# Kernel tuning notes

Hardware: AMD Instinct MI355X
Metric: run time of the kernel (lower is better)

Reference implementation:

```python
import jax, jax.numpy as jnp
import numpy as np

B, S, HID = 1, 2048, 3072
NH, NKV, HD = 24, 8, 128
ROT = 96
OP = NH * HD + 2 * NKV * HD
MASK_VALUE = -jnp.finfo(jnp.float32).max


def setup_inputs() -> dict:
    key = jax.random.key(0)
    k1, k2, k3, k4, k5 = jax.random.split(key, 5)
    hidden_states = jax.random.normal(k1, (B, S, HID), dtype=jnp.float32)
    # rotary embeddings: use actual cos/sin of rope angles for realism
    inv_freq = 1.0 / (10000.0 ** (jnp.arange(0, ROT, 2, dtype=jnp.float32) / ROT))
    t = jnp.arange(S, dtype=jnp.float32)
    freqs = jnp.outer(t, inv_freq)  # [S, ROT/2]
    emb = jnp.concatenate([freqs, freqs], axis=-1)  # [S, ROT]
    cos = jnp.broadcast_to(jnp.cos(emb)[None], (B, S, ROT))
    sin = jnp.broadcast_to(jnp.sin(emb)[None], (B, S, ROT))
    attention_mask = jnp.ones((B, S), dtype=bool)
    w_qkv = jax.random.normal(k2, (OP, HID), dtype=jnp.float32) * (HID ** -0.5)
    w_o = jax.random.normal(k3, (HID, HID), dtype=jnp.float32) * (HID ** -0.5)
    return {"hidden_states": hidden_states, "cos": cos, "sin": sin,
            "attention_mask": attention_mask, "w_qkv": w_qkv, "w_o": w_o}


def rotate_half(x):
    x1, x2 = jnp.split(x, 2, axis=-1)
    return jnp.concatenate([-x2, x1], axis=-1)


def apply_rope(q, k, cos, sin):
    # cos/sin: [B, S, ROT] -> [B, 1, S, ROT]
    cos = cos[:, None]
    sin = sin[:, None]
    rd = cos.shape[-1]
    q_rot, q_pass = q[..., :rd], q[..., rd:]
    k_rot, k_pass = k[..., :rd], k[..., rd:]
    q = jnp.concatenate([q_rot * cos + rotate_half(q_rot) * sin, q_pass], axis=-1)
    k = jnp.concatenate([k_rot * cos + rotate_half(k_rot) * sin, k_pass], axis=-1)
    return q, k


def reference(hidden_states, cos, sin, attention_mask, w_qkv, w_o):
    b, n, _ = hidden_states.shape
    qkv = hidden_states @ w_qkv.T  # [B, S, OP]
    q, k, v = jnp.split(qkv, [NH * HD, NH * HD + NKV * HD], axis=-1)
    # b n (h d) -> b h n d
    q = q.reshape(b, n, NH, HD).transpose(0, 2, 1, 3)
    k = k.reshape(b, n, NKV, HD).transpose(0, 2, 1, 3)
    v = v.reshape(b, n, NKV, HD).transpose(0, 2, 1, 3)
    q, k = apply_rope(q, k, cos, sin)
    q = q * (HD ** -0.5)
    n_rep = NH // NKV
    if n_rep > 1:
        k = jnp.repeat(k, n_rep, axis=1)
        v = jnp.repeat(v, n_rep, axis=1)
    sim = jnp.einsum('bhid,bhjd->bhij', q, k)
    causal = jnp.triu(jnp.ones((n, n), dtype=bool), k=1)
    sim = jnp.where(causal, MASK_VALUE, sim)
    sim = jnp.where(~attention_mask[:, None, None, :], MASK_VALUE, sim)
    attn = jax.nn.softmax(sim.astype(jnp.float32), axis=-1).astype(v.dtype)
    out = jnp.einsum('bhij,bhjd->bhid', attn, v)
    out = out.transpose(0, 2, 1, 3).reshape(b, n, NH * HD)  # b h n d -> b n (h d)
    return out @ w_o.T
```

## Files before the change

kernel.cpp:

```cpp
#include <hip/hip_runtime.h>

typedef unsigned short u16;
typedef unsigned int u32;
typedef __bf16 bf16x8 __attribute__((ext_vector_type(8)));
typedef float f32x4 __attribute__((ext_vector_type(4)));

#define S_LEN 2048
#define HIDDEN 3072
#define NHEADS 24
#define NKVH 8
#define HDIM 128
#define QKVW 5120
#define QKLD 4096
#define PSTR 80

__device__ __forceinline__ u16 f2bf(float f) {
  u32 u = __float_as_uint(f);
  u32 r = (u + 0x7fffu + ((u >> 16) & 1u)) >> 16;
  return (u16)r;
}
__device__ __forceinline__ float bf2f(u16 h) { return __uint_as_float(((u32)h) << 16); }

__device__ __forceinline__ void gload_lds16(const void* g, void* l) {
  __builtin_amdgcn_global_load_lds((const __attribute__((address_space(1))) void*)g,
                                   (__attribute__((address_space(3))) void*)l, 16, 0, 0);
}

__global__ void cast4(const float4* __restrict__ in, uint2* __restrict__ out, int n4) {
  int i = blockIdx.x * blockDim.x + threadIdx.x;
  if (i >= n4) return;
  float4 f = in[i];
  uint2 o;
  o.x = ((u32)f2bf(f.y) << 16) | f2bf(f.x);
  o.y = ((u32)f2bf(f.w) << 16) | f2bf(f.z);
  out[i] = o;
}

__global__ __launch_bounds__(512, 2) void gemm256(const u16* __restrict__ A,
                                                  const u16* __restrict__ B,
                                                  u16* __restrict__ Cb,
                                                  u16* __restrict__ vtg) {
  __shared__ u16 lds[4][13312];
  const int tid = threadIdx.x;
  const int w = tid >> 6, lane = tid & 63;
  const int wm = w & 3, wn = w >> 2;
  const int l15 = lane & 15, qd = lane >> 4;
  const int K = 3072;
  const int m0 = ((int)blockIdx.x & 7) * 256;
  const int n0 = ((int)blockIdx.x >> 3) * 160;

  size_t offA[2], offB[2];
  int ldsA[2], ldsB[2];
#pragma unroll
  for (int it = 0; it < 2; ++it) {
    int CH = w * 128 + it * 64 + lane;
    int rp = CH >> 3, sl = CH & 7;
    int lin = sl ^ (rp & 7);
    int r = (rp << 1) | (lin >> 2), q = lin & 3;
    offA[it] = (size_t)(m0 + r) * K + q * 8;
    ldsA[it] = (w * 128 + it * 64) * 8;
  }
#pragma unroll
  for (int it = 0; it < 2; ++it) {
    int CH = it * 512 + w * 64 + lane;
    int rp = CH >> 3, sl = CH & 7;
    int lin = sl ^ (rp & 7);
    int r = (rp << 1) | (lin >> 2), q = lin & 3;
    offB[it] = (size_t)(n0 + r) * K + q * 8;
    ldsB[it] = 8192 + (it * 512 + w * 64) * 8;
  }

  int chA[4], chB[5];
#pragma unroll
  for (int i = 0; i < 4; ++i) {
    int r = wm * 64 + i * 16 + l15;
    chA[i] = ((r >> 1) * 8 + ((((r & 1) << 2) | qd) ^ ((r >> 1) & 7))) * 8;
  }
#pragma unroll
  for (int j = 0; j < 5; ++j) {
    int r = wn * 80 + j * 16 + l15;
    chB[j] = 8192 + ((r >> 1) * 8 + ((((r & 1) << 2) | qd) ^ ((r >> 1) & 7))) * 8;
  }

  f32x4 acc[4][5] = {};

  auto stage = [&](int s, int k0) {
    gload_lds16(A + offA[0] + k0, &lds[s][ldsA[0]]);
    gload_lds16(A + offA[1] + k0, &lds[s][ldsA[1]]);
    gload_lds16(B + offB[0] + k0, &lds[s][ldsB[0]]);
    if (w < 2) gload_lds16(B + offB[1] + k0, &lds[s][ldsB[1]]);
  };

  auto tile = [&](int s, int kpf, bool pf) {
    if (pf) stage((kpf >> 5) & 3, kpf);
    bf16x8 a[4], b[5];
#pragma unroll
    for (int i = 0; i < 4; ++i) a[i] = *(const bf16x8*)&lds[s][chA[i]];
#pragma unroll
    for (int j = 0; j < 5; ++j) b[j] = *(const bf16x8*)&lds[s][chB[j]];
    __builtin_amdgcn_s_setprio(1);
#pragma unroll
    for (int i = 0; i < 4; ++i)
#pragma unroll
      for (int j = 0; j < 5; ++j)
        acc[i][j] = __builtin_amdgcn_mfma_f32_16x16x32_bf16(a[i], b[j], acc[i][j], 0, 0, 0);
    __builtin_amdgcn_s_setprio(0);
  };

  stage(0, 0);
  stage(1, 32);
  stage(2, 64);
  if (w < 2) asm volatile("s_waitcnt vmcnt(8)" ::: "memory");
  else       asm volatile("s_waitcnt vmcnt(6)" ::: "memory");
  __builtin_amdgcn_s_barrier();

  for (int t = 0; t < 93; ++t) {
    tile(t & 3, (t + 3) * 32, true);
    if (w < 2) asm volatile("s_waitcnt vmcnt(8)" ::: "memory");
    else       asm volatile("s_waitcnt vmcnt(6)" ::: "memory");
    __builtin_amdgcn_s_barrier();
  }
  tile(1, 0, false);
  if (w < 2) asm volatile("s_waitcnt vmcnt(4)" ::: "memory");
  else       asm volatile("s_waitcnt vmcnt(3)" ::: "memory");
  __builtin_amdgcn_s_barrier();
  tile(2, 0, false);
  asm volatile("s_waitcnt vmcnt(0)" ::: "memory");
  __builtin_amdgcn_s_barrier();
  tile(3, 0, false);

#pragma unroll
  for (int j = 0; j < 5; ++j) {
    const int nf = n0 + wn * 80 + j * 16;
    if (nf >= 4096) {
#pragma unroll
      for (int i = 0; i < 4; ++i) {
        int nv = nf - 4096 + l15;
        int m = m0 + wm * 64 + i * 16 + qd * 4;
        uint2 p;
        p.x = ((u32)f2bf(acc[i][j][1]) << 16) | f2bf(acc[i][j][0]);
        p.y = ((u32)f2bf(acc[i][j][3]) << 16) | f2bf(acc[i][j][2]);
        *(uint2*)&vtg[(size_t)nv * S_LEN + m] = p;
      }
    } else {
#pragma unroll
      for (int i = 0; i < 4; ++i)
#pragma unroll
        for (int r = 0; r < 4; ++r) {
          int m = m0 + wm * 64 + i * 16 + qd * 4 + r;
          Cb[(size_t)m * QKLD + nf + l15] = f2bf(acc[i][j][r]);
        }
    }
  }
}

__global__ __launch_bounds__(512, 2) void gemm2k(const u16* __restrict__ A,
                                                 const u16* __restrict__ B,
                                                 float* __restrict__ C) {
  __shared__ u16 lds[4][10240];
  const int tid = threadIdx.x;
  const int w = tid >> 6, lane = tid & 63;
  const int wm = w & 1, wn = w >> 1;
  const int l15 = lane & 15, qd = lane >> 4;
  const int K = 3072;
  const int xcd = (int)blockIdx.x & 7, idx = (int)blockIdx.x >> 3;
  const int m0 = ((xcd & 1) * 8 + (idx & 7)) * 128;
  const int n0 = ((xcd >> 1) * 4 + (idx >> 3)) * 192;

  size_t offA, offB[2];
  int ldsAo, ldsB[2];
  {
    int CH = w * 64 + lane;
    int rp = CH >> 3, sl = CH & 7;
    int lin = sl ^ (rp & 7);
    int r = (rp << 1) | (lin >> 2), q = lin & 3;
    offA = (size_t)(m0 + r) * K + q * 8;
    ldsAo = (w * 64) * 8;
  }
#pragma unroll
  for (int it = 0; it < 2; ++it) {
    int CHb = (w < 4) ? (w * 128 + it * 64) : (512 + (w - 4) * 64);
    int CH = CHb + lane;
    int rp = CH >> 3, sl = CH & 7;
    int lin = sl ^ (rp & 7);
    int r = (rp << 1) | (lin >> 2), q = lin & 3;
    offB[it] = (size_t)(n0 + r) * K + q * 8;
    ldsB[it] = 4096 + CHb * 8;
  }

  int chA[4], chB[3];
#pragma unroll
  for (int i = 0; i < 4; ++i) {
    int r = wm * 64 + i * 16 + l15;
    chA[i] = ((r >> 1) * 8 + ((((r & 1) << 2) | qd) ^ ((r >> 1) & 7))) * 8;
  }
#pragma unroll
  for (int j = 0; j < 3; ++j) {
    int r = wn * 48 + j * 16 + l15;
    chB[j] = 4096 + ((r >> 1) * 8 + ((((r & 1) << 2) | qd) ^ ((r >> 1) & 7))) * 8;
  }

  f32x4 acc[4][3] = {};

  auto stage = [&](int s, int k0) {
    gload_lds16(A + offA + k0, &lds[s][ldsAo]);
    gload_lds16(B + offB[0] + k0, &lds[s][ldsB[0]]);
    if (w < 4) gload_lds16(B + offB[1] + k0, &lds[s][ldsB[1]]);
  };

  auto tile = [&](int s, int kpf, bool pf) {
    if (pf) stage((kpf >> 5) & 3, kpf);
    bf16x8 a[4], b[3];
#pragma unroll
    for (int i = 0; i < 4; ++i) a[i] = *(const bf16x8*)&lds[s][chA[i]];
#pragma unroll
    for (int j = 0; j < 3; ++j) b[j] = *(const bf16x8*)&lds[s][chB[j]];
    __builtin_amdgcn_s_setprio(1);
#pragma unroll
    for (int i = 0; i < 4; ++i)
#pragma unroll
      for (int j = 0; j < 3; ++j)
        acc[i][j] = __builtin_amdgcn_mfma_f32_16x16x32_bf16(a[i], b[j], acc[i][j], 0, 0, 0);
    __builtin_amdgcn_s_setprio(0);
  };

  stage(0, 0);
  stage(1, 32);
  stage(2, 64);
  if (w < 4) asm volatile("s_waitcnt vmcnt(6)" ::: "memory");
  else       asm volatile("s_waitcnt vmcnt(4)" ::: "memory");
  __builtin_amdgcn_s_barrier();

  for (int t = 0; t < 93; ++t) {
    tile(t & 3, (t + 3) * 32, true);
    if (w < 4) asm volatile("s_waitcnt vmcnt(6)" ::: "memory");
    else       asm volatile("s_waitcnt vmcnt(4)" ::: "memory");
    __builtin_amdgcn_s_barrier();
  }
  tile(1, 0, false);
  if (w < 4) asm volatile("s_waitcnt vmcnt(3)" ::: "memory");
  else       asm volatile("s_waitcnt vmcnt(2)" ::: "memory");
  __builtin_amdgcn_s_barrier();
  tile(2, 0, false);
  asm volatile("s_waitcnt vmcnt(0)" ::: "memory");
  __builtin_amdgcn_s_barrier();
  tile(3, 0, false);

#pragma unroll
  for (int i = 0; i < 4; ++i)
#pragma unroll
    for (int j = 0; j < 3; ++j)
#pragma unroll
      for (int r = 0; r < 4; ++r) {
        int m = m0 + wm * 64 + i * 16 + qd * 4 + r;
        int n = n0 + wn * 48 + j * 16 + l15;
        C[(size_t)m * HIDDEN + n] = acc[i][j][r];
      }
}

__global__ __launch_bounds__(128) void rope_kernel(u16* __restrict__ qkv,
                                                   const float* __restrict__ cosb,
                                                   const float* __restrict__ sinb) {
  const int s = blockIdx.x;
  const int hh = blockIdx.y;
  const int d = threadIdx.x;
  const bool isq = hh < NHEADS;
  const size_t base = (size_t)s * QKLD + (isq ? hh * HDIM : HIDDEN + (hh - NHEADS) * HDIM);
  const float scale = 0.08838834764831845f;
  if (d < 48) {
    float x1 = bf2f(qkv[base + d]), x2 = bf2f(qkv[base + d + 48]);
    float c1 = cosb[s * 96 + d], s1 = sinb[s * 96 + d];
    float c2 = cosb[s * 96 + d + 48], s2 = sinb[s * 96 + d + 48];
    float o1 = x1 * c1 - x2 * s1;
    float o2 = x2 * c2 + x1 * s2;
    if (isq) { o1 *= scale; o2 *= scale; }
    qkv[base + d] = f2bf(o1);
    qkv[base + d + 48] = f2bf(o2);
  } else if (d >= 96 && isq) {
    qkv[base + d] = f2bf(bf2f(qkv[base + d]) * scale);
  }
}

__global__ __launch_bounds__(256) void flash_kernel(const u16* __restrict__ qkv,
                                                    const u16* __restrict__ vtg,
                                                    u16* __restrict__ ao) {
  __shared__ u16 Ks[4][64 * 32];
  __shared__ u16 Vt[128 * PSTR];
  __shared__ u16 Ps[64 * PSTR];
  const int bid = blockIdx.x;
  const int g = bid & 255, kk3 = bid >> 8;
  const int rank = (kk3 == 1) ? (kk3 << 8) + (255 - g) : (kk3 << 8) + g;
  const int h = rank % NHEADS;
  const int qi = 31 - rank / NHEADS;
  const int q0 = qi * 64;
  const int hkv = h / 3;
  const int tid = threadIdx.x;
  const int w = tid >> 6, lane = tid & 63;
  const int l15 = lane & 15, qd = lane >> 4;

  const int krp = lane >> 3, ksl = lane & 7;
  const int klin = ksl ^ (krp & 7);
  const int kR = (krp << 1) | (klin >> 2);
  const int kQ = klin & 3;
  const int kslot = ((l15 >> 1) * 8 + ((((l15 & 1) << 2) | qd) ^ ((l15 >> 1) & 7))) * 8;

  bf16x8 qf[4];
#pragma unroll
  for (int kk = 0; kk < 4; ++kk)
    qf[kk] = *(const bf16x8*)&qkv[(size_t)(q0 + w * 16 + l15) * QKLD + h * HDIM + kk * 32 + qd * 8];

  f32x4 o[8] = {};
  float lrow[4] = {0.f, 0.f, 0.f, 0.f};

  const u16* vb = vtg + (size_t)hkv * HDIM * S_LEN;
  const int vd = tid >> 3;
  const int vkv = (tid & 7) * 8;

  for (int kv0 = 0; kv0 <= q0; kv0 += 64) {
    __syncthreads();
#pragma unroll
    for (int t = 0; t < 4; ++t)
      gload_lds16(qkv + (size_t)(kv0 + t * 16 + kR) * QKLD + HIDDEN + hkv * HDIM + w * 32 + kQ * 8,
                  &Ks[w][t * 512]);
#pragma unroll
    for (int it = 0; it < 4; ++it) {
      int d = it * 32 + vd;
      uint4 vv = *(const uint4*)&vb[(size_t)d * S_LEN + kv0 + vkv];
      *(uint4*)&Vt[d * PSTR + vkv] = vv;
    }
    __syncthreads();

    f32x4 sc[4] = {};
#pragma unroll
    for (int j = 0; j < 4; ++j)
#pragma unroll
      for (int kk = 0; kk < 4; ++kk) {
        bf16x8 kf = *(const bf16x8*)&Ks[kk][j * 512 + kslot];
        sc[j] = __builtin_amdgcn_mfma_f32_16x16x32_bf16(qf[kk], kf, sc[j], 0, 0, 0);
      }

    if (kv0 == q0) {
#pragma unroll
      for (int j = 0; j < 4; ++j)
#pragma unroll
        for (int r = 0; r < 4; ++r) {
          int row = w * 16 + qd * 4 + r;
          int col = j * 16 + l15;
          if (col > row) sc[j][r] = -1.0e30f;
        }
    }

#pragma unroll
    for (int j = 0; j < 4; ++j)
#pragma unroll
      for (int r = 0; r < 4; ++r) sc[j][r] = __expf(sc[j][r]);
#pragma unroll
    for (int r = 0; r < 4; ++r)
      lrow[r] += (sc[0][r] + sc[1][r]) + (sc[2][r] + sc[3][r]);

#pragma unroll
    for (int j = 0; j < 4; ++j)
#pragma unroll
      for (int r = 0; r < 4; ++r)
        Ps[(w * 16 + qd * 4 + r) * PSTR + j * 16 + l15] = f2bf(sc[j][r]);
    asm volatile("s_waitcnt lgkmcnt(0)" ::: "memory");

    bf16x8 pf[2];
#pragma unroll
    for (int kk = 0; kk < 2; ++kk)
      pf[kk] = *(const bf16x8*)&Ps[(w * 16 + l15) * PSTR + kk * 32 + qd * 8];
#pragma unroll
    for (int jn = 0; jn < 8; ++jn)
#pragma unroll
      for (int kk = 0; kk < 2; ++kk) {
        bf16x8 vf = *(const bf16x8*)&Vt[(jn * 16 + l15) * PSTR + kk * 32 + qd * 8];
        o[jn] = __builtin_amdgcn_mfma_f32_16x16x32_bf16(pf[kk], vf, o[jn], 0, 0, 0);
      }
  }

  float rinv[4];
#pragma unroll
  for (int r = 0; r < 4; ++r) {
    float s = lrow[r];
#pragma unroll
    for (int d = 1; d < 16; d <<= 1) s += __shfl_xor(s, d, 64);
    rinv[r] = 1.0f / s;
  }
#pragma unroll
  for (int jn = 0; jn < 8; ++jn)
#pragma unroll
    for (int r = 0; r < 4; ++r) {
      int row = q0 + w * 16 + qd * 4 + r;
      ao[(size_t)row * HIDDEN + h * HDIM + jn * 16 + l15] = f2bf(o[jn][r] * rinv[r]);
    }
}

extern "C" void kernel_launch(void* const* d_in, const int* in_sizes, int n_in,
                              void* d_out, int out_size, void* d_ws, size_t ws_size,
                              hipStream_t stream) {
  (void)in_sizes; (void)n_in; (void)out_size; (void)ws_size;
  const float* hs   = (const float*)d_in[0];
  const float* cosb = (const float*)d_in[1];
  const float* sinb = (const float*)d_in[2];
  const float* wqkv = (const float*)d_in[4];
  const float* wo   = (const float*)d_in[5];
  float* out = (float*)d_out;
  char* ws = (char*)d_ws;

  u16* hB   = (u16*)ws;
  u16* wB   = (u16*)(ws + 12582912);
  u16* qkvB = (u16*)(ws + 44040192);
  u16* vtgB = (u16*)(ws + 60817408);
  u16* aoB  = hB;
  u16* woB  = wB;

  cast4<<<6144, 256, 0, stream>>>((const float4*)hs, (uint2*)hB, 1572864);
  cast4<<<15360, 256, 0, stream>>>((const float4*)wqkv, (uint2*)wB, 3932160);
  gemm256<<<256, 512, 0, stream>>>(hB, wB, qkvB, vtgB);
  cast4<<<9216, 256, 0, stream>>>((const float4*)wo, (uint2*)woB, 2359296);
  rope_kernel<<<dim3(2048, 32), 128, 0, stream>>>(qkvB, cosb, sinb);
  flash_kernel<<<768, 256, 0, stream>>>(qkvB, vtgB, aoB);
  gemm2k<<<256, 512, 0, stream>>>(aoB, woB, out);
}
```

Measured before the change: 351.0 us.

## Merge pre-GEMM cast launches, widen cast per-thread work, batch rope heads per block

Merges the two fp32-to-bf16 casts for hidden states and QKV weights into one launch, with each thread converting two float4s. The w_o cast also handles two float4s per thread. The rope kernel now runs one 256-thread block per sequence position, looping over all 32 heads and loading cos/sin once per position instead of once per head. This cuts launch count and tiny-block scheduling overhead, in exchange for fewer, larger blocks and less parallel slack in the rope kernel.

```diff
diff --git a/kernel.cpp b/kernel.cpp
--- a/kernel.cpp
+++ b/kernel.cpp
@@ -26,14 +26,31 @@
                                    (__attribute__((address_space(3))) void*)l, 16, 0, 0);
 }
 
-__global__ void cast4(const float4* __restrict__ in, uint2* __restrict__ out, int n4) {
-  int i = blockIdx.x * blockDim.x + threadIdx.x;
-  if (i >= n4) return;
-  float4 f = in[i];
+__device__ __forceinline__ uint2 cvt4(float4 f) {
   uint2 o;
   o.x = ((u32)f2bf(f.y) << 16) | f2bf(f.x);
   o.y = ((u32)f2bf(f.w) << 16) | f2bf(f.z);
-  out[i] = o;
+  return o;
+}
+
+__global__ void cast8(const float4* __restrict__ in, uint2* __restrict__ out, int n4) {
+  int i = (blockIdx.x * blockDim.x + threadIdx.x) * 2;
+  if (i >= n4) return;
+  out[i] = cvt4(in[i]);
+  out[i + 1] = cvt4(in[i + 1]);
+}
+
+__global__ void cast_pre(const float4* __restrict__ hs, uint2* __restrict__ hB,
+                         const float4* __restrict__ wq, uint2* __restrict__ wB) {
+  int i = (blockIdx.x * blockDim.x + threadIdx.x) * 2;
+  if (i < 1572864) {
+    hB[i] = cvt4(hs[i]);
+    hB[i + 1] = cvt4(hs[i + 1]);
+  } else {
+    int j = i - 1572864;
+    wB[j] = cvt4(wq[j]);
+    wB[j + 1] = cvt4(wq[j + 1]);
+  }
 }
 
 __global__ __launch_bounds__(512, 2) void gemm256(const u16* __restrict__ A,
@@ -258,26 +275,38 @@
       }
 }
 
-__global__ __launch_bounds__(128) void rope_kernel(u16* __restrict__ qkv,
+__global__ __launch_bounds__(256) void rope_kernel(u16* __restrict__ qkv,
                                                    const float* __restrict__ cosb,
                                                    const float* __restrict__ sinb) {
   const int s = blockIdx.x;
-  const int hh = blockIdx.y;
-  const int d = threadIdx.x;
-  const bool isq = hh < NHEADS;
-  const size_t base = (size_t)s * QKLD + (isq ? hh * HDIM : HIDDEN + (hh - NHEADS) * HDIM);
+  const int d = threadIdx.x & 127;
+  const int h0 = threadIdx.x >> 7;
   const float scale = 0.08838834764831845f;
+
+  float c1 = 0.f, s1 = 0.f, c2 = 0.f, s2 = 0.f;
   if (d < 48) {
-    float x1 = bf2f(qkv[base + d]), x2 = bf2f(qkv[base + d + 48]);
-    float c1 = cosb[s * 96 + d], s1 = sinb[s * 96 + d];
-    float c2 = cosb[s * 96 + d + 48], s2 = sinb[s * 96 + d + 48];
-    float o1 = x1 * c1 - x2 * s1;
-    float o2 = x2 * c2 + x1 * s2;
-    if (isq) { o1 *= scale; o2 *= scale; }
-    qkv[base + d] = f2bf(o1);
-    qkv[base + d + 48] = f2bf(o2);
-  } else if (d >= 96 && isq) {
-    qkv[base + d] = f2bf(bf2f(qkv[base + d]) * scale);
+    c1 = cosb[s * 96 + d];
+    s1 = sinb[s * 96 + d];
+    c2 = cosb[s * 96 + d + 48];
+    s2 = sinb[s * 96 + d + 48];
+  }
+  const size_t srow = (size_t)s * QKLD;
+
+#pragma unroll
+  for (int it = 0; it < 16; ++it) {
+    const int hh = h0 + it * 2;
+    const bool isq = hh < NHEADS;
+    const size_t base = srow + (isq ? hh * HDIM : HIDDEN + (hh - NHEADS) * HDIM);
+    if (d < 48) {
+      float x1 = bf2f(qkv[base + d]), x2 = bf2f(qkv[base + d + 48]);
+      float o1 = x1 * c1 - x2 * s1;
+      float o2 = x2 * c2 + x1 * s2;
+      if (isq) { o1 *= scale; o2 *= scale; }
+      qkv[base + d] = f2bf(o1);
+      qkv[base + d + 48] = f2bf(o2);
+    } else if (d >= 96 && isq) {
+      qkv[base + d] = f2bf(bf2f(qkv[base + d]) * scale);
+    }
   }
 }
 
@@ -414,11 +443,11 @@
   u16* aoB  = hB;
   u16* woB  = wB;
 
-  cast4<<<6144, 256, 0, stream>>>((const float4*)hs, (uint2*)hB, 1572864);
-  cast4<<<15360, 256, 0, stream>>>((const float4*)wqkv, (uint2*)wB, 3932160);
+  cast_pre<<<10752, 256, 0, stream>>>((const float4*)hs, (uint2*)hB,
+                                      (const float4*)wqkv, (uint2*)wB);
   gemm256<<<256, 512, 0, stream>>>(hB, wB, qkvB, vtgB);
-  cast4<<<9216, 256, 0, stream>>>((const float4*)wo, (uint2*)woB, 2359296);
-  rope_kernel<<<dim3(2048, 32), 128, 0, stream>>>(qkvB, cosb, sinb);
+  cast8<<<4608, 256, 0, stream>>>((const float4*)wo, (uint2*)woB, 2359296);
+  rope_kernel<<<2048, 256, 0, stream>>>(qkvB, cosb, sinb);
   flash_kernel<<<768, 256, 0, stream>>>(qkvB, vtgB, aoB);
   gemm2k<<<256, 512, 0, stream>>>(aoB, woB, out);
 }
```

New measurement: 336.9 us. 4.0% less time.
